# Kernel optimization log

Measured on AMD Instinct MI355X. Metric: run time of the kernel, lower is better.

## Reference

```python
import jax, jax.numpy as jnp
import numpy as np

N_QUBITS = 12   # data qubits; device has 3*n wires but ancillas provably stay in a product state
N_LAYERS = 6
BATCH = 768


def _apply_1q(state, gate, wire):
    """state: (B,)+(2,)*n complex; gate: (2,2) shared or (B,2,2) per-sample."""
    state = jnp.moveaxis(state, 1 + wire, -1)
    if gate.ndim == 3:
        state = jnp.einsum('b...i,bji->b...j', state, gate)
    else:
        state = jnp.einsum('b...i,ji->b...j', state, gate)
    return jnp.moveaxis(state, -1, 1 + wire)


def _apply_cnot(state, control, target):
    state = jnp.moveaxis(state, (1 + control, 1 + target), (-2, -1))
    state = jnp.stack([state[..., 0, :], state[..., 1, ::-1]], axis=-2)
    return jnp.moveaxis(state, (-2, -1), (1 + control, 1 + target))


def _forward(x, params):
    B, n = x.shape
    dim = 2 ** n
    state = jnp.zeros((B, dim), jnp.complex64).at[:, 0].set(1.0)
    state = state.reshape((B,) + (2,) * n)
    # angle embedding: RX(x[:, i]) on data qubit i (per-sample batched gates)
    c = jnp.cos(x / 2).astype(jnp.complex64)          # (B, n)
    s = (-1j * jnp.sin(x / 2)).astype(jnp.complex64)  # (B, n)
    for i in range(n):
        g = jnp.stack([jnp.stack([c[:, i], s[:, i]], -1),
                       jnp.stack([s[:, i], c[:, i]], -1)], -2)  # (B,2,2)
        state = _apply_1q(state, g, i)
    # variational layers: Rot(phi, theta, omega) = RZ(omega) RY(theta) RZ(phi), then CNOT chain
    for l in range(params.shape[0]):
        for q in range(n):
            phi, theta, omega = params[l, q, 0], params[l, q, 1], params[l, q, 2]
            ct, st = jnp.cos(theta / 2), jnp.sin(theta / 2)
            ep = jnp.exp(-0.5j * (phi + omega))   # e^{-i(phi+omega)/2}
            em = jnp.exp(0.5j * (phi - omega))    # e^{ i(phi-omega)/2}
            g = jnp.stack([jnp.stack([ep * ct, -em * st]),
                           jnp.stack([jnp.conj(em) * st, jnp.conj(ep) * ct])])
        
            state = _apply_1q(state, g, q)
        for q in range(n - 1):
            state = _apply_cnot(state, q, q + 1)
    # <Z_i> for each data qubit via a single probs @ signs matmul
    probs = jnp.abs(state.reshape(B, dim)) ** 2
    bits = (jnp.arange(dim)[:, None] >> jnp.arange(n - 1, -1, -1)[None, :]) & 1
    signs = (1.0 - 2.0 * bits).astype(probs.dtype)     # (dim, n)
    exps = probs @ signs                               # (B, n)
    # readout-error mitigation: calibration matrix from ideal simulator SPAM runs
    # (ideal <Z_j> for basis state with qubit i flipped -> (Z+1)/2 = ones - eye)
    M = jnp.ones((n, n), probs.dtype) - jnp.eye(n, dtype=probs.dtype)
    calib = jnp.linalg.pinv(M)
    mitigated = ((exps + 1.0) * 0.5) @ calib.T
    return 2.0 * mitigated - 1.0


def setup_inputs() -> dict:
    key = jax.random.key(0)
    k1, k2 = jax.random.split(key)
    x = jax.random.normal(k1, (BATCH, N_QUBITS), jnp.float32)
    params = jax.random.normal(k2, (N_LAYERS, N_QUBITS, 3), jnp.float32)
    return {"x": x, "params": params}


def reference(x, params):
    return _forward(x, params)
```

## Files before the change

### kernel.cpp

```cpp
#include <hip/hip_runtime.h>

#define NQ 12
#define DIM 4096
#define NL 6
#define THREADS 512
#define BATCH 768

struct M12 { unsigned c[12]; };
constexpr unsigned mapv(const M12& m, unsigned v) {
    unsigned r = 0;
    for (int i = 0; i < 12; ++i) if ((v >> i) & 1) r ^= m.c[i];
    return r;
}
constexpr M12 ident() { M12 m{}; for (int i = 0; i < 12; ++i) m.c[i] = 1u << i; return m; }
constexpr M12 mmul(const M12& a, const M12& b) { M12 r{}; for (int i = 0; i < 12; ++i) r.c[i] = mapv(a, b.c[i]); return r; }
constexpr M12 Gmat()  { M12 m{}; for (int i = 0; i < 12; ++i) m.c[i] = (1u << i) | (i ? (1u << (i - 1)) : 0u); return m; }
constexpr M12 Gimat() { M12 m{}; for (int i = 0; i < 12; ++i) m.c[i] = (2u << i) - 1u; return m; }
constexpr M12 Tmat()  { M12 m = ident(); for (int i = 0; i < 3; ++i) { m.c[i] = 1u << (9 + i); m.c[9 + i] = 1u << i; } return m; }
constexpr M12 Gpow(int n)  { M12 r = ident(); for (int i = 0; i < n; ++i) r = mmul(Gmat(),  r); return r; }
constexpr M12 Gipow(int n) { M12 r = ident(); for (int i = 0; i < n; ++i) r = mmul(Gimat(), r); return r; }
constexpr M12 Lam(int k)    { return (k & 1) ? mmul(Gpow(k - 1), Tmat()) : Gpow(k); }
constexpr M12 LamInv(int k) { return (k & 1) ? mmul(Tmat(), Gipow(k - 1)) : Gipow(k); }
constexpr int par(unsigned v) { int c = 0; for (int b = 0; b < 12; ++b) c ^= (v >> b) & 1; return c; }
constexpr unsigned mask_of(int lam, int p, int k) { return mapv(LamInv(k), mapv(Gpow(lam), 1u << p)); }
constexpr unsigned role_of(int lam, int p, int k) {
    unsigned f = 0;
    for (int b = 0; b < 12; ++b)
        if ((mapv(Gipow(lam), mapv(Lam(k), 1u << b)) >> p) & 1) f |= 1u << b;
    return f;
}
constexpr unsigned kap(unsigned h) { return ((h & 7u) << 9) | (h >> 3); }
struct Off8  { unsigned v[8]; };
struct Col12 { unsigned v[12]; };
constexpr Off8 offs_of(int k) {
    M12 R = mmul(LamInv(k - 1), Lam(k));
    Off8 o{};
    for (unsigned j = 0; j < 8; ++j) o.v[j] = kap(mapv(R, j));
    return o;
}
constexpr Col12 cols_of(int k) {
    M12 R = mmul(LamInv(k - 1), Lam(k));
    Col12 c{};
    for (int i = 0; i < 12; ++i) c.v[i] = kap(mapv(R, 1u << i));
    return c;
}

__device__ __forceinline__ float2 crow(float2 c0, float2 a, float2 c1, float2 b) {
    float2 r;
    r.x = c0.x * a.x - c0.y * a.y + c1.x * b.x - c1.y * b.y;
    r.y = c0.x * a.y + c0.y * a.x + c1.x * b.y + c1.y * b.x;
    return r;
}
template<int CTRL> __device__ __forceinline__ float dppf(float v) {
    return __int_as_float(__builtin_amdgcn_update_dpp(0, __float_as_int(v), CTRL, 0xF, 0xF, true));
}
template<int XM> __device__ __forceinline__ float bxf(float v) {
    if constexpr (XM == 1)      return dppf<0xB1>(v);
    else if constexpr (XM == 2) return dppf<0x4E>(v);
    else if constexpr (XM == 3) return dppf<0x1B>(v);
    else if constexpr (XM < 32) return __int_as_float(__builtin_amdgcn_ds_swizzle(__float_as_int(v), (XM << 10) | 0x1F));
    else                        return __shfl_xor(v, XM, 64);
}
template<int XM> __device__ __forceinline__ float2 bx2(float2 v) { return make_float2(bxf<XM>(v.x), bxf<XM>(v.y)); }

template<int LAM, int P, int K>
__device__ __forceinline__ void pass(float2 (&amp)[8], const float* __restrict__ gw, const int lane) {
    constexpr unsigned MU = mask_of(LAM, P, K);
    constexpr unsigned FV = role_of(LAM, P, K);
    static_assert(MU != 0 && (MU >> 9) == 0, "mask touches wave bits");
    static_assert((FV >> 9) == 0, "role touches wave bits");
    static_assert(par(MU & FV) == 1, "pair not split by role");
    constexpr int MJ = MU & 7, ML = (int)(MU >> 3);
    constexpr int FJ = FV & 7, FL = (int)(FV >> 3);
    constexpr int GI = (LAM * NQ + (11 - P)) * 8;
    const float2 g00 = make_float2(gw[GI + 0], gw[GI + 1]);
    const float2 g01 = make_float2(gw[GI + 2], gw[GI + 3]);
    const float2 g10 = make_float2(gw[GI + 4], gw[GI + 5]);
    const float2 g11 = make_float2(gw[GI + 6], gw[GI + 7]);
    if constexpr (ML == 0) {
        float2 Oda = g00, Ooa = g01, Odb = g11, Oob = g10;
        if constexpr (FL != 0) {
            const bool lf = (__popc(lane & FL) & 1) != 0;
            Oda = lf ? g11 : g00; Ooa = lf ? g10 : g01;
            Odb = lf ? g00 : g11; Oob = lf ? g01 : g10;
        }
        #pragma unroll
        for (int j = 0; j < 8; ++j) {
            if ((__builtin_popcount((unsigned)(FJ & j)) & 1) == 0) {
                const int jb = j ^ MJ;
                const float2 a = amp[j], b = amp[jb];
                amp[j]  = crow(Oda, a, Ooa, b);
                amp[jb] = crow(Odb, b, Oob, a);
            }
        }
    } else {
        float2 pv[8];
        #pragma unroll
        for (int j = 0; j < 8; ++j) pv[j] = bx2<ML>(amp[j ^ MJ]);
        if constexpr (FL == 0) {
            #pragma unroll
            for (int j = 0; j < 8; ++j) {
                constexpr_bool_hack:;
                const bool r = (__builtin_popcount((unsigned)(FJ & j)) & 1) != 0;
                amp[j] = crow(r ? g11 : g00, amp[j], r ? g10 : g01, pv[j]);
            }
        } else {
            const bool lf = (__popc(lane & FL) & 1) != 0;
            const float2 O0d = lf ? g11 : g00, O0o = lf ? g10 : g01;
            const float2 O1d = lf ? g00 : g11, O1o = lf ? g01 : g10;
            #pragma unroll
            for (int j = 0; j < 8; ++j) {
                const bool r = (__builtin_popcount((unsigned)(FJ & j)) & 1) != 0;
                amp[j] = crow(r ? O1d : O0d, amp[j], r ? O1o : O0o, pv[j]);
            }
        }
    }
}

template<int K>
__device__ __forceinline__ unsigned tbase(const int tid) {
    constexpr Col12 C = cols_of(K);
    unsigned r = 0;
    #pragma unroll
    for (int i = 3; i < 12; ++i)
        if ((tid >> (i - 3)) & 1) r ^= C.v[i];
    return r;
}
template<int K>
__device__ __forceinline__ void transit(float2 (&amp)[8], float2* __restrict__ st,
                                        const int tid, const unsigned baseT, const unsigned baseG) {
    if constexpr (K > 1) __syncthreads();
    #pragma unroll
    for (int j = 0; j < 8; ++j) st[(j << 9) | tid] = amp[j];
    __syncthreads();
    constexpr Off8 OF = offs_of(K);
    const unsigned base = (K & 1) ? baseT : baseG;
    #pragma unroll
    for (int j = 0; j < 8; ++j) amp[j] = st[base ^ OF.v[j]];
}

template<int B>
__device__ __forceinline__ void rstage(float& v, float (&D)[6], float& a9, float& a10, float& a11) {
    constexpr int XM = 1 << B;
    const float sv = bxf<XM>(v);
    D[B] = v - sv;
    v += sv;
    #pragma unroll
    for (int c = 0; c < B; ++c) D[c] += bxf<XM>(D[c]);
    a9 += bxf<XM>(a9); a10 += bxf<XM>(a10); a11 += bxf<XM>(a11);
}

__global__ void setup_kernel(const float* __restrict__ x, const float* __restrict__ params,
                             float* __restrict__ ws) {
    const int t = blockIdx.x * 256 + threadIdx.x;
    if (t < NL * NQ) {
        const float phi = params[t * 3 + 0], th = params[t * 3 + 1], om = params[t * 3 + 2];
        float ct, stt, ca, sa, cb, sb;
        __sincosf(0.5f * th, &stt, &ct);
        __sincosf(0.5f * (phi + om), &sa, &ca);
        __sincosf(0.5f * (phi - om), &sb, &cb);
        float* g = ws + t * 8;
        g[0] =  ca * ct;  g[1] = -sa * ct;
        g[2] = -cb * stt; g[3] = -sb * stt;
        g[4] =  cb * stt; g[5] = -sb * stt;
        g[6] =  ca * ct;  g[7] =  sa * ct;
    }
    if (t < BATCH * NQ) {
        const int bb = t / NQ, i = t - bb * NQ;
        float s, c;
        __sincosf(0.5f * x[t], &s, &c);
        ws[1024 + bb * 32 + i]      = c;
        ws[1024 + bb * 32 + 16 + i] = s;
    }
}

__global__ __launch_bounds__(THREADS, 6)
void qsim_kernel(const float* __restrict__ ws, float* __restrict__ out) {
    __shared__ float2 st[DIM];
    __shared__ float red[8 * 10];
    __shared__ float ev[NQ];

    const int b = blockIdx.x;
    const int tid = threadIdx.x;
    const int lane = tid & 63;
    const int wave = tid >> 6;
    const float* __restrict__ gw = ws;
    const float* __restrict__ cs = ws + 1024 + b * 32;

    const unsigned baseT = tbase<1>(tid);
    const unsigned baseG = tbase<2>(tid);

    float rt = 1.0f;
    #pragma unroll
    for (int i = 0; i < 9; ++i) {
        const bool bit = (tid >> (8 - i)) & 1;
        rt *= bit ? cs[16 + i] : cs[i];
    }
    const int pt = __popc((unsigned)tid & 0x1FFu);
    float2 amp[8];
    #pragma unroll
    for (int j = 0; j < 8; ++j) {
        float v = rt;
        v *= (j & 4) ? cs[16 + 9]  : cs[9];
        v *= (j & 2) ? cs[16 + 10] : cs[10];
        v *= (j & 1) ? cs[16 + 11] : cs[11];
        const int ph = (pt + __builtin_popcount((unsigned)j)) & 3;
        amp[j].x = (ph == 0) ? v : (ph == 2) ? -v : 0.0f;
        amp[j].y = (ph == 1) ? -v : (ph == 3) ? v : 0.0f;
    }

    pass<0,0,0>(amp, gw, lane); pass<0,1,0>(amp, gw, lane); pass<0,2,0>(amp, gw, lane);
    pass<0,3,0>(amp, gw, lane); pass<0,4,0>(amp, gw, lane); pass<0,5,0>(amp, gw, lane);
    pass<0,6,0>(amp, gw, lane); pass<0,7,0>(amp, gw, lane); pass<0,8,0>(amp, gw, lane);
    transit<1>(amp, st, tid, baseT, baseG);
    pass<0,9,1>(amp, gw, lane); pass<0,10,1>(amp, gw, lane); pass<0,11,1>(amp, gw, lane);
    pass<1,11,1>(amp, gw, lane); pass<1,10,1>(amp, gw, lane); pass<1,9,1>(amp, gw, lane);
    pass<1,8,1>(amp, gw, lane);  pass<1,7,1>(amp, gw, lane);  pass<1,6,1>(amp, gw, lane);
    pass<1,5,1>(amp, gw, lane);  pass<1,4,1>(amp, gw, lane);
    transit<2>(amp, st, tid, baseT, baseG);
    pass<1,0,2>(amp, gw, lane); pass<1,1,2>(amp, gw, lane); pass<1,2,2>(amp, gw, lane); pass<1,3,2>(amp, gw, lane);
    pass<2,0,2>(amp, gw, lane); pass<2,1,2>(amp, gw, lane); pass<2,2,2>(amp, gw, lane);
    pass<2,3,2>(amp, gw, lane); pass<2,4,2>(amp, gw, lane); pass<2,5,2>(amp, gw, lane);
    pass<2,6,2>(amp, gw, lane); pass<2,7,2>(amp, gw, lane); pass<2,8,2>(amp, gw, lane);
    transit<3>(amp, st, tid, baseT, baseG);
    pass<2,9,3>(amp, gw, lane); pass<2,10,3>(amp, gw, lane); pass<2,11,3>(amp, gw, lane);
    pass<3,11,3>(amp, gw, lane); pass<3,10,3>(amp, gw, lane); pass<3,9,3>(amp, gw, lane);
    pass<3,8,3>(amp, gw, lane);  pass<3,7,3>(amp, gw, lane);  pass<3,6,3>(amp, gw, lane);
    pass<3,5,3>(amp, gw, lane);  pass<3,4,3>(amp, gw, lane);
    transit<4>(amp, st, tid, baseT, baseG);
    pass<3,0,4>(amp, gw, lane); pass<3,1,4>(amp, gw, lane); pass<3,2,4>(amp, gw, lane); pass<3,3,4>(amp, gw, lane);
    pass<4,0,4>(amp, gw, lane); pass<4,1,4>(amp, gw, lane); pass<4,2,4>(amp, gw, lane);
    pass<4,3,4>(amp, gw, lane); pass<4,4,4>(amp, gw, lane); pass<4,5,4>(amp, gw, lane);
    pass<4,6,4>(amp, gw, lane); pass<4,7,4>(amp, gw, lane); pass<4,8,4>(amp, gw, lane);
    transit<5>(amp, st, tid, baseT, baseG);
    pass<4,9,5>(amp, gw, lane); pass<4,10,5>(amp, gw, lane); pass<4,11,5>(amp, gw, lane);
    pass<5,11,5>(amp, gw, lane); pass<5,10,5>(amp, gw, lane); pass<5,9,5>(amp, gw, lane);
    pass<5,8,5>(amp, gw, lane);  pass<5,7,5>(amp, gw, lane);  pass<5,6,5>(amp, gw, lane);
    pass<5,5,5>(amp, gw, lane);  pass<5,4,5>(amp, gw, lane);
    transit<6>(amp, st, tid, baseT, baseG);
    pass<5,0,6>(amp, gw, lane); pass<5,1,6>(amp, gw, lane); pass<5,2,6>(amp, gw, lane); pass<5,3,6>(amp, gw, lane);

    float p8[8];
    #pragma unroll
    for (int j = 0; j < 8; ++j) p8[j] = amp[j].x * amp[j].x + amp[j].y * amp[j].y;
    const float t01 = p8[0] + p8[1], d01 = p8[0] - p8[1];
    const float t23 = p8[2] + p8[3], d23 = p8[2] - p8[3];
    const float t45 = p8[4] + p8[5], d45 = p8[4] - p8[5];
    const float t67 = p8[6] + p8[7], d67 = p8[6] - p8[7];
    const float s03 = t01 + t23, s47 = t45 + t67;
    float S   = s03 + s47;
    float a11 = (d01 + d23) + (d45 + d67);
    float a10 = (t01 - t23) + (t45 - t67);
    float a9  = s03 - s47;
    float D[6];
    rstage<0>(S, D, a9, a10, a11); rstage<1>(S, D, a9, a10, a11);
    rstage<2>(S, D, a9, a10, a11); rstage<3>(S, D, a9, a10, a11);
    rstage<4>(S, D, a9, a10, a11); rstage<5>(S, D, a9, a10, a11);
    if (lane == 0) {
        float* rw = red + wave * 10;
        rw[0] = S;
        #pragma unroll
        for (int c = 0; c < 6; ++c) rw[1 + c] = D[c];
        rw[7] = a9; rw[8] = a10; rw[9] = a11;
    }
    __syncthreads();
    if (tid < NQ) {
        float e = 0.0f;
        #pragma unroll
        for (int w = 0; w < 8; ++w) {
            const float* rw = red + w * 10;
            float s;
            if (tid == 0)      s = ((w >> 2) & 1) ? -rw[0] : rw[0];
            else if (tid == 1) s = ((w >> 1) & 1) ? -rw[0] : rw[0];
            else if (tid == 2) s = ((w >> 0) & 1) ? -rw[0] : rw[0];
            else if (tid < 9)  s = rw[1 + (8 - tid)];
            else               s = rw[7 + (tid - 9)];
            e += s;
        }
        ev[tid] = e;
    }
    __syncthreads();
    if (tid < NQ) {
        float Sm = 0.0f;
        #pragma unroll
        for (int i = 0; i < NQ; ++i) Sm += ev[i];
        out[b * NQ + tid] = (Sm + 12.0f) * (1.0f / 11.0f) - ev[tid] - 2.0f;
    }
}

extern "C" void kernel_launch(void* const* d_in, const int* in_sizes, int n_in,
                              void* d_out, int out_size, void* d_ws, size_t ws_size,
                              hipStream_t stream) {
    const float* x      = (const float*)d_in[0];
    const float* params = (const float*)d_in[1];
    float* ws  = (float*)d_ws;
    float* out = (float*)d_out;
    setup_kernel<<<dim3(36), dim3(256), 0, stream>>>(x, params, ws);
    qsim_kernel<<<dim3(BATCH), dim3(THREADS), 0, stream>>>(ws, out);
}
```

Baseline: 106.0 us.

## Restructure simulator to 256 threads with 16 amplitudes each and packed-FP32 gates

Switches the per-sample statevector kernel from 512 threads holding 8 amplitudes to 256 threads holding 16. A new qubit-permutation schedule lets each half-layer apply 4 gates in registers and 2 via DPP lane swaps, with one shared-memory transpose between half-layers. Complex amplitudes are packed as doubles and multiplied with v_pk_mul/v_pk_fma inline assembly. The shared-memory layout gets an XOR swizzle to reduce bank conflicts. This aims to cut shuffle, LDS and sync overhead per gate, but raises register pressure (launch bounds go from 6 to 4) and leaves fewer waves per block.

```diff
diff --git a/kernel.cpp b/kernel.cpp
--- a/kernel.cpp
+++ b/kernel.cpp
@@ -3,7 +3,7 @@
 #define NQ 12
 #define DIM 4096
 #define NL 6
-#define THREADS 512
+#define THREADS 256
 #define BATCH 768
 
 struct M12 { unsigned c[12]; };
@@ -16,40 +16,102 @@
 constexpr M12 mmul(const M12& a, const M12& b) { M12 r{}; for (int i = 0; i < 12; ++i) r.c[i] = mapv(a, b.c[i]); return r; }
 constexpr M12 Gmat()  { M12 m{}; for (int i = 0; i < 12; ++i) m.c[i] = (1u << i) | (i ? (1u << (i - 1)) : 0u); return m; }
 constexpr M12 Gimat() { M12 m{}; for (int i = 0; i < 12; ++i) m.c[i] = (2u << i) - 1u; return m; }
-constexpr M12 Tmat()  { M12 m = ident(); for (int i = 0; i < 3; ++i) { m.c[i] = 1u << (9 + i); m.c[9 + i] = 1u << i; } return m; }
-constexpr M12 Gpow(int n)  { M12 r = ident(); for (int i = 0; i < n; ++i) r = mmul(Gmat(),  r); return r; }
-constexpr M12 Gipow(int n) { M12 r = ident(); for (int i = 0; i < n; ++i) r = mmul(Gimat(), r); return r; }
-constexpr M12 Lam(int k)    { return (k & 1) ? mmul(Gpow(k - 1), Tmat()) : Gpow(k); }
-constexpr M12 LamInv(int k) { return (k & 1) ? mmul(Tmat(), Gipow(k - 1)) : Gipow(k); }
-constexpr int par(unsigned v) { int c = 0; for (int b = 0; b < 12; ++b) c ^= (v >> b) & 1; return c; }
-constexpr unsigned mask_of(int lam, int p, int k) { return mapv(LamInv(k), mapv(Gpow(lam), 1u << p)); }
+constexpr M12 Smat()  { M12 m{}; for (int i = 0; i < 12; ++i) m.c[i] = (i < 6) ? (1u << (i + 6)) : (1u << (i - 6)); return m; }
+struct Pow7 { M12 p[7]; };
+constexpr Pow7 mkpow(const M12 g) { Pow7 t{}; t.p[0] = ident(); for (int i = 1; i < 7; ++i) t.p[i] = mmul(g, t.p[i - 1]); return t; }
+constexpr Pow7 GP  = mkpow(Gmat());
+constexpr Pow7 GIP = mkpow(Gimat());
+struct LamT { M12 l[13]; };
+constexpr LamT mklam() {
+    LamT t{};
+    for (int k = 0; k < 12; ++k) t.l[k] = (k & 1) ? GP.p[k >> 1] : mmul(GP.p[k >> 1], Smat());
+    t.l[12] = GP.p[6];
+    return t;
+}
+constexpr LamT mklami() {
+    LamT t{};
+    for (int k = 0; k < 12; ++k) t.l[k] = (k & 1) ? GIP.p[k >> 1] : mmul(Smat(), GIP.p[k >> 1]);
+    t.l[12] = GIP.p[6];
+    return t;
+}
+constexpr LamT LAMT  = mklam();
+constexpr LamT LAMIT = mklami();
+constexpr bool eqm(const M12& a, const M12& b) { for (int i = 0; i < 12; ++i) if (a.c[i] != b.c[i]) return false; return true; }
+constexpr unsigned mask_of(int lam, int p, int k) { return mapv(LAMIT.l[k], mapv(GP.p[lam], 1u << p)); }
 constexpr unsigned role_of(int lam, int p, int k) {
     unsigned f = 0;
     for (int b = 0; b < 12; ++b)
-        if ((mapv(Gipow(lam), mapv(Lam(k), 1u << b)) >> p) & 1) f |= 1u << b;
+        if ((mapv(GIP.p[lam], mapv(LAMT.l[k], 1u << b)) >> p) & 1) f |= 1u << b;
     return f;
 }
-constexpr unsigned kap(unsigned h) { return ((h & 7u) << 9) | (h >> 3); }
-struct Off8  { unsigned v[8]; };
-struct Col12 { unsigned v[12]; };
-constexpr Off8 offs_of(int k) {
-    M12 R = mmul(LamInv(k - 1), Lam(k));
-    Off8 o{};
-    for (unsigned j = 0; j < 8; ++j) o.v[j] = kap(mapv(R, j));
-    return o;
-}
-constexpr Col12 cols_of(int k) {
-    M12 R = mmul(LamInv(k - 1), Lam(k));
-    Col12 c{};
-    for (int i = 0; i < 12; ++i) c.v[i] = kap(mapv(R, 1u << i));
-    return c;
-}
-
-__device__ __forceinline__ float2 crow(float2 c0, float2 a, float2 c1, float2 b) {
-    float2 r;
-    r.x = c0.x * a.x - c0.y * a.y + c1.x * b.x - c1.y * b.y;
-    r.y = c0.x * a.y + c0.y * a.x + c1.x * b.y + c1.y * b.x;
-    return r;
+constexpr bool check_layer(int L) {
+    for (int p = 0; p < 12; ++p) {
+        const int k = (p >= 6) ? 2 * L : 2 * L + 1;
+        const unsigned exp_ = (p >= 6) ? (1u << (p - 6)) : (1u << p);
+        if (mask_of(L, p, k) != exp_) return false;
+        if (role_of(L, p, k) != exp_) return false;
+    }
+    return true;
+}
+static_assert(check_layer(0), "layer0 masks/roles not unit cheap bits");
+static_assert(check_layer(1), "layer1");
+static_assert(check_layer(2), "layer2");
+static_assert(check_layer(3), "layer3");
+static_assert(check_layer(4), "layer4");
+static_assert(check_layer(5), "layer5");
+constexpr M12 Rk(int k) { return mmul(LAMIT.l[k - 1], LAMT.l[k]); }
+constexpr M12 R_S  = Smat();
+constexpr M12 R_GS = mmul(Gmat(), Smat());
+constexpr M12 R_G  = Gmat();
+static_assert(eqm(Rk(1), R_S) && eqm(Rk(3), R_S) && eqm(Rk(11), R_S), "T1 != S");
+static_assert(eqm(Rk(2), R_GS) && eqm(Rk(10), R_GS), "T2 != G*S");
+static_assert(eqm(Rk(12), R_G), "T3 != G");
+
+constexpr unsigned kap(unsigned h) {
+    const unsigned cell = ((h & 15u) << 8) | (h >> 4);
+    return cell ^ ((cell >> 8) & 15u) ^ (((cell >> 6) & 3u) << 4);
+}
+struct Off16 { unsigned v[16]; };
+struct Col8  { unsigned v[8]; };
+constexpr Off16 roff(const M12& R) { Off16 o{}; for (unsigned j = 0; j < 16; ++j) o.v[j] = kap(mapv(R, j)); return o; }
+constexpr Col8  rcol(const M12& R) { Col8 c{}; for (int i = 0; i < 8; ++i) c.v[i] = kap(mapv(R, 1u << (4 + i))); return c; }
+constexpr Off16 OFF_S = roff(R_S), OFF_GS = roff(R_GS), OFF_G = roff(R_G);
+constexpr Col8  COL_S = rcol(R_S), COL_GS = rcol(R_GS), COL_G = rcol(R_G);
+
+__device__ __forceinline__ double pkmul_s(double c, double a) {
+    double r;
+    asm("v_pk_mul_f32 %0, %1, %2 op_sel:[0,0] op_sel_hi:[0,1]\n\t"
+        "v_pk_fma_f32 %0, %1, %2, %0 op_sel:[1,1,0] op_sel_hi:[1,0,1] neg_lo:[1,0,0]"
+        : "=&v"(r) : "s"(c), "v"(a));
+    return r;
+}
+__device__ __forceinline__ double pkfma_s(double c, double a, double d) {
+    double r;
+    asm("v_pk_fma_f32 %0, %1, %2, %3 op_sel:[0,0,0] op_sel_hi:[0,1,1]\n\t"
+        "v_pk_fma_f32 %0, %1, %2, %0 op_sel:[1,1,0] op_sel_hi:[1,0,1] neg_lo:[1,0,0]"
+        : "=&v"(r) : "s"(c), "v"(a), "v"(d));
+    return r;
+}
+__device__ __forceinline__ double pkmul_v(double c, double a) {
+    double r;
+    asm("v_pk_mul_f32 %0, %1, %2 op_sel:[0,0] op_sel_hi:[0,1]\n\t"
+        "v_pk_fma_f32 %0, %1, %2, %0 op_sel:[1,1,0] op_sel_hi:[1,0,1] neg_lo:[1,0,0]"
+        : "=&v"(r) : "v"(c), "v"(a));
+    return r;
+}
+__device__ __forceinline__ double pkfma_v(double c, double a, double d) {
+    double r;
+    asm("v_pk_fma_f32 %0, %1, %2, %3 op_sel:[0,0,0] op_sel_hi:[0,1,1]\n\t"
+        "v_pk_fma_f32 %0, %1, %2, %0 op_sel:[1,1,0] op_sel_hi:[1,0,1] neg_lo:[1,0,0]"
+        : "=&v"(r) : "v"(c), "v"(a), "v"(d));
+    return r;
+}
+
+template<int CTRL>
+__device__ __forceinline__ double dpp64(double v) {
+    const int lo = __builtin_amdgcn_update_dpp(0, __double2loint(v), CTRL, 0xF, 0xF, true);
+    const int hi = __builtin_amdgcn_update_dpp(0, __double2hiint(v), CTRL, 0xF, 0xF, true);
+    return __hiloint2double(hi, lo);
 }
 template<int CTRL> __device__ __forceinline__ float dppf(float v) {
     return __int_as_float(__builtin_amdgcn_update_dpp(0, __float_as_int(v), CTRL, 0xF, 0xF, true));
@@ -57,97 +119,87 @@
 template<int XM> __device__ __forceinline__ float bxf(float v) {
     if constexpr (XM == 1)      return dppf<0xB1>(v);
     else if constexpr (XM == 2) return dppf<0x4E>(v);
-    else if constexpr (XM == 3) return dppf<0x1B>(v);
     else if constexpr (XM < 32) return __int_as_float(__builtin_amdgcn_ds_swizzle(__float_as_int(v), (XM << 10) | 0x1F));
     else                        return __shfl_xor(v, XM, 64);
 }
-template<int XM> __device__ __forceinline__ float2 bx2(float2 v) { return make_float2(bxf<XM>(v.x), bxf<XM>(v.y)); }
-
-template<int LAM, int P, int K>
-__device__ __forceinline__ void pass(float2 (&amp)[8], const float* __restrict__ gw, const int lane) {
-    constexpr unsigned MU = mask_of(LAM, P, K);
-    constexpr unsigned FV = role_of(LAM, P, K);
-    static_assert(MU != 0 && (MU >> 9) == 0, "mask touches wave bits");
-    static_assert((FV >> 9) == 0, "role touches wave bits");
-    static_assert(par(MU & FV) == 1, "pair not split by role");
-    constexpr int MJ = MU & 7, ML = (int)(MU >> 3);
-    constexpr int FJ = FV & 7, FL = (int)(FV >> 3);
-    constexpr int GI = (LAM * NQ + (11 - P)) * 8;
-    const float2 g00 = make_float2(gw[GI + 0], gw[GI + 1]);
-    const float2 g01 = make_float2(gw[GI + 2], gw[GI + 3]);
-    const float2 g10 = make_float2(gw[GI + 4], gw[GI + 5]);
-    const float2 g11 = make_float2(gw[GI + 6], gw[GI + 7]);
-    if constexpr (ML == 0) {
-        float2 Oda = g00, Ooa = g01, Odb = g11, Oob = g10;
-        if constexpr (FL != 0) {
-            const bool lf = (__popc(lane & FL) & 1) != 0;
-            Oda = lf ? g11 : g00; Ooa = lf ? g10 : g01;
-            Odb = lf ? g00 : g11; Oob = lf ? g01 : g10;
+
+template<int RB>
+__device__ __forceinline__ void regpassPK(double (&amp)[16], const double* __restrict__ g) {
+    const double g00 = g[0], g01 = g[1], g10 = g[2], g11 = g[3];
+    #pragma unroll
+    for (int j = 0; j < 16; ++j)
+        if (!(j & (1 << RB))) {
+            const int jb = j | (1 << RB);
+            const double a = amp[j], b2 = amp[jb];
+            amp[j]  = pkfma_s(g01, b2, pkmul_s(g00, a));
+            amp[jb] = pkfma_s(g10, a,  pkmul_s(g11, b2));
         }
-        #pragma unroll
-        for (int j = 0; j < 8; ++j) {
-            if ((__builtin_popcount((unsigned)(FJ & j)) & 1) == 0) {
-                const int jb = j ^ MJ;
-                const float2 a = amp[j], b = amp[jb];
-                amp[j]  = crow(Oda, a, Ooa, b);
-                amp[jb] = crow(Odb, b, Oob, a);
-            }
-        }
-    } else {
-        float2 pv[8];
-        #pragma unroll
-        for (int j = 0; j < 8; ++j) pv[j] = bx2<ML>(amp[j ^ MJ]);
-        if constexpr (FL == 0) {
-            #pragma unroll
-            for (int j = 0; j < 8; ++j) {
-                constexpr_bool_hack:;
-                const bool r = (__builtin_popcount((unsigned)(FJ & j)) & 1) != 0;
-                amp[j] = crow(r ? g11 : g00, amp[j], r ? g10 : g01, pv[j]);
-            }
-        } else {
-            const bool lf = (__popc(lane & FL) & 1) != 0;
-            const float2 O0d = lf ? g11 : g00, O0o = lf ? g10 : g01;
-            const float2 O1d = lf ? g00 : g11, O1o = lf ? g01 : g10;
-            #pragma unroll
-            for (int j = 0; j < 8; ++j) {
-                const bool r = (__builtin_popcount((unsigned)(FJ & j)) & 1) != 0;
-                amp[j] = crow(r ? O1d : O0d, amp[j], r ? O1o : O0o, pv[j]);
-            }
-        }
-    }
-}
-
-template<int K>
-__device__ __forceinline__ unsigned tbase(const int tid) {
-    constexpr Col12 C = cols_of(K);
+}
+template<int XM>
+__device__ __forceinline__ void dpppassPK(double (&amp)[16], const double* __restrict__ g, const int lane) {
+    constexpr int CTRL = (XM == 1) ? 0xB1 : 0x4E;
+    const bool side = (lane & XM) != 0;
+    const double cA = side ? g[3] : g[0];
+    const double cB = side ? g[2] : g[1];
+    #pragma unroll
+    for (int j = 0; j < 16; ++j) {
+        const double r = dpp64<CTRL>(amp[j]);
+        amp[j] = pkfma_v(cB, r, pkmul_v(cA, amp[j]));
+    }
+}
+
+template<int L>
+__device__ __forceinline__ void epochA(double (&amp)[16], const double* __restrict__ gd, const int lane) {
+    const double* gL = gd + L * 48;
+    regpassPK<0>(amp, gL + 5 * 4);
+    regpassPK<1>(amp, gL + 4 * 4);
+    regpassPK<2>(amp, gL + 3 * 4);
+    regpassPK<3>(amp, gL + 2 * 4);
+    dpppassPK<1>(amp, gL + 1 * 4, lane);
+    dpppassPK<2>(amp, gL + 0 * 4, lane);
+}
+template<int L>
+__device__ __forceinline__ void epochB(double (&amp)[16], const double* __restrict__ gd, const int lane) {
+    const double* gL = gd + L * 48;
+    regpassPK<0>(amp, gL + 11 * 4);
+    regpassPK<1>(amp, gL + 10 * 4);
+    regpassPK<2>(amp, gL +  9 * 4);
+    regpassPK<3>(amp, gL +  8 * 4);
+    dpppassPK<1>(amp, gL + 7 * 4, lane);
+    dpppassPK<2>(amp, gL + 6 * 4, lane);
+}
+
+template<int RSEL, bool FIRST>
+__device__ __forceinline__ void transit(double (&amp)[16], double* __restrict__ st,
+                                        const unsigned wbase, const unsigned rbase) {
+    if constexpr (!FIRST) __syncthreads();
+    #pragma unroll
+    for (int j = 0; j < 16; ++j)
+        st[wbase ^ (unsigned)((j << 8) ^ j)] = amp[j];
+    __syncthreads();
+    constexpr Off16 OF = (RSEL == 0) ? OFF_S : (RSEL == 1) ? OFF_GS : OFF_G;
+    #pragma unroll
+    for (int j = 0; j < 16; ++j) amp[j] = st[rbase ^ OF.v[j]];
+}
+template<int RSEL>
+__device__ __forceinline__ unsigned rbase_of(const int tid) {
+    constexpr Col8 C = (RSEL == 0) ? COL_S : (RSEL == 1) ? COL_GS : COL_G;
     unsigned r = 0;
     #pragma unroll
-    for (int i = 3; i < 12; ++i)
-        if ((tid >> (i - 3)) & 1) r ^= C.v[i];
-    return r;
-}
-template<int K>
-__device__ __forceinline__ void transit(float2 (&amp)[8], float2* __restrict__ st,
-                                        const int tid, const unsigned baseT, const unsigned baseG) {
-    if constexpr (K > 1) __syncthreads();
-    #pragma unroll
-    for (int j = 0; j < 8; ++j) st[(j << 9) | tid] = amp[j];
-    __syncthreads();
-    constexpr Off8 OF = offs_of(K);
-    const unsigned base = (K & 1) ? baseT : baseG;
-    #pragma unroll
-    for (int j = 0; j < 8; ++j) amp[j] = st[base ^ OF.v[j]];
+    for (int i = 0; i < 8; ++i) if ((tid >> i) & 1) r ^= C.v[i];
+    return r;
 }
 
 template<int B>
-__device__ __forceinline__ void rstage(float& v, float (&D)[6], float& a9, float& a10, float& a11) {
+__device__ __forceinline__ void rstage(float& S, float (&D)[6], float (&Bv)[4]) {
     constexpr int XM = 1 << B;
-    const float sv = bxf<XM>(v);
-    D[B] = v - sv;
-    v += sv;
+    const float sv = bxf<XM>(S);
+    D[B] = S - sv;
+    S += sv;
     #pragma unroll
     for (int c = 0; c < B; ++c) D[c] += bxf<XM>(D[c]);
-    a9 += bxf<XM>(a9); a10 += bxf<XM>(a10); a11 += bxf<XM>(a11);
+    #pragma unroll
+    for (int q = 0; q < 4; ++q) Bv[q] += bxf<XM>(Bv[q]);
 }
 
 __global__ void setup_kernel(const float* __restrict__ x, const float* __restrict__ params,
@@ -174,107 +226,101 @@
     }
 }
 
-__global__ __launch_bounds__(THREADS, 6)
+__global__ __launch_bounds__(THREADS, 4)
 void qsim_kernel(const float* __restrict__ ws, float* __restrict__ out) {
-    __shared__ float2 st[DIM];
-    __shared__ float red[8 * 10];
+    __shared__ double st[DIM];
+    __shared__ float red[4 * 11];
     __shared__ float ev[NQ];
 
     const int b = blockIdx.x;
     const int tid = threadIdx.x;
     const int lane = tid & 63;
     const int wave = tid >> 6;
-    const float* __restrict__ gw = ws;
-    const float* __restrict__ cs = ws + 1024 + b * 32;
-
-    const unsigned baseT = tbase<1>(tid);
-    const unsigned baseG = tbase<2>(tid);
+    const double* __restrict__ gd = (const double*)ws;
+    const float*  __restrict__ cs = ws + 1024 + b * 32;
+
+    const unsigned wbase = (unsigned)tid ^ (((unsigned)tid & 0xC0u) >> 2);
+    const unsigned rbS  = rbase_of<0>(tid);
+    const unsigned rbGS = rbase_of<1>(tid);
+    const unsigned rbG  = rbase_of<2>(tid);
 
     float rt = 1.0f;
-    #pragma unroll
-    for (int i = 0; i < 9; ++i) {
-        const bool bit = (tid >> (8 - i)) & 1;
-        rt *= bit ? cs[16 + i] : cs[i];
-    }
-    const int pt = __popc((unsigned)tid & 0x1FFu);
-    float2 amp[8];
-    #pragma unroll
-    for (int j = 0; j < 8; ++j) {
+    rt *= ((tid >> 1) & 1) ? cs[16 + 0]  : cs[0];
+    rt *= ((tid >> 0) & 1) ? cs[16 + 1]  : cs[1];
+    rt *= ((tid >> 7) & 1) ? cs[16 + 6]  : cs[6];
+    rt *= ((tid >> 6) & 1) ? cs[16 + 7]  : cs[7];
+    rt *= ((tid >> 5) & 1) ? cs[16 + 8]  : cs[8];
+    rt *= ((tid >> 4) & 1) ? cs[16 + 9]  : cs[9];
+    rt *= ((tid >> 3) & 1) ? cs[16 + 10] : cs[10];
+    rt *= ((tid >> 2) & 1) ? cs[16 + 11] : cs[11];
+    const int pt = __popc((unsigned)tid & 0xFFu);
+
+    double amp[16];
+    #pragma unroll
+    for (int j = 0; j < 16; ++j) {
         float v = rt;
-        v *= (j & 4) ? cs[16 + 9]  : cs[9];
-        v *= (j & 2) ? cs[16 + 10] : cs[10];
-        v *= (j & 1) ? cs[16 + 11] : cs[11];
+        v *= (j & 8) ? cs[16 + 2] : cs[2];
+        v *= (j & 4) ? cs[16 + 3] : cs[3];
+        v *= (j & 2) ? cs[16 + 4] : cs[4];
+        v *= (j & 1) ? cs[16 + 5] : cs[5];
         const int ph = (pt + __builtin_popcount((unsigned)j)) & 3;
-        amp[j].x = (ph == 0) ? v : (ph == 2) ? -v : 0.0f;
-        amp[j].y = (ph == 1) ? -v : (ph == 3) ? v : 0.0f;
-    }
-
-    pass<0,0,0>(amp, gw, lane); pass<0,1,0>(amp, gw, lane); pass<0,2,0>(amp, gw, lane);
-    pass<0,3,0>(amp, gw, lane); pass<0,4,0>(amp, gw, lane); pass<0,5,0>(amp, gw, lane);
-    pass<0,6,0>(amp, gw, lane); pass<0,7,0>(amp, gw, lane); pass<0,8,0>(amp, gw, lane);
-    transit<1>(amp, st, tid, baseT, baseG);
-    pass<0,9,1>(amp, gw, lane); pass<0,10,1>(amp, gw, lane); pass<0,11,1>(amp, gw, lane);
-    pass<1,11,1>(amp, gw, lane); pass<1,10,1>(amp, gw, lane); pass<1,9,1>(amp, gw, lane);
-    pass<1,8,1>(amp, gw, lane);  pass<1,7,1>(amp, gw, lane);  pass<1,6,1>(amp, gw, lane);
-    pass<1,5,1>(amp, gw, lane);  pass<1,4,1>(amp, gw, lane);
-    transit<2>(amp, st, tid, baseT, baseG);
-    pass<1,0,2>(amp, gw, lane); pass<1,1,2>(amp, gw, lane); pass<1,2,2>(amp, gw, lane); pass<1,3,2>(amp, gw, lane);
-    pass<2,0,2>(amp, gw, lane); pass<2,1,2>(amp, gw, lane); pass<2,2,2>(amp, gw, lane);
-    pass<2,3,2>(amp, gw, lane); pass<2,4,2>(amp, gw, lane); pass<2,5,2>(amp, gw, lane);
-    pass<2,6,2>(amp, gw, lane); pass<2,7,2>(amp, gw, lane); pass<2,8,2>(amp, gw, lane);
-    transit<3>(amp, st, tid, baseT, baseG);
-    pass<2,9,3>(amp, gw, lane); pass<2,10,3>(amp, gw, lane); pass<2,11,3>(amp, gw, lane);
-    pass<3,11,3>(amp, gw, lane); pass<3,10,3>(amp, gw, lane); pass<3,9,3>(amp, gw, lane);
-    pass<3,8,3>(amp, gw, lane);  pass<3,7,3>(amp, gw, lane);  pass<3,6,3>(amp, gw, lane);
-    pass<3,5,3>(amp, gw, lane);  pass<3,4,3>(amp, gw, lane);
-    transit<4>(amp, st, tid, baseT, baseG);
-    pass<3,0,4>(amp, gw, lane); pass<3,1,4>(amp, gw, lane); pass<3,2,4>(amp, gw, lane); pass<3,3,4>(amp, gw, lane);
-    pass<4,0,4>(amp, gw, lane); pass<4,1,4>(amp, gw, lane); pass<4,2,4>(amp, gw, lane);
-    pass<4,3,4>(amp, gw, lane); pass<4,4,4>(amp, gw, lane); pass<4,5,4>(amp, gw, lane);
-    pass<4,6,4>(amp, gw, lane); pass<4,7,4>(amp, gw, lane); pass<4,8,4>(amp, gw, lane);
-    transit<5>(amp, st, tid, baseT, baseG);
-    pass<4,9,5>(amp, gw, lane); pass<4,10,5>(amp, gw, lane); pass<4,11,5>(amp, gw, lane);
-    pass<5,11,5>(amp, gw, lane); pass<5,10,5>(amp, gw, lane); pass<5,9,5>(amp, gw, lane);
-    pass<5,8,5>(amp, gw, lane);  pass<5,7,5>(amp, gw, lane);  pass<5,6,5>(amp, gw, lane);
-    pass<5,5,5>(amp, gw, lane);  pass<5,4,5>(amp, gw, lane);
-    transit<6>(amp, st, tid, baseT, baseG);
-    pass<5,0,6>(amp, gw, lane); pass<5,1,6>(amp, gw, lane); pass<5,2,6>(amp, gw, lane); pass<5,3,6>(amp, gw, lane);
-
-    float p8[8];
-    #pragma unroll
-    for (int j = 0; j < 8; ++j) p8[j] = amp[j].x * amp[j].x + amp[j].y * amp[j].y;
-    const float t01 = p8[0] + p8[1], d01 = p8[0] - p8[1];
-    const float t23 = p8[2] + p8[3], d23 = p8[2] - p8[3];
-    const float t45 = p8[4] + p8[5], d45 = p8[4] - p8[5];
-    const float t67 = p8[6] + p8[7], d67 = p8[6] - p8[7];
-    const float s03 = t01 + t23, s47 = t45 + t67;
-    float S   = s03 + s47;
-    float a11 = (d01 + d23) + (d45 + d67);
-    float a10 = (t01 - t23) + (t45 - t67);
-    float a9  = s03 - s47;
+        const float re = (ph == 0) ? v : (ph == 2) ? -v : 0.0f;
+        const float im = (ph == 1) ? -v : (ph == 3) ? v : 0.0f;
+        amp[j] = __hiloint2double(__float_as_int(im), __float_as_int(re));
+    }
+
+    epochA<0>(amp, gd, lane); transit<0, true >(amp, st, wbase, rbS);
+    epochB<0>(amp, gd, lane); transit<1, false>(amp, st, wbase, rbGS);
+    epochA<1>(amp, gd, lane); transit<0, false>(amp, st, wbase, rbS);
+    epochB<1>(amp, gd, lane); transit<1, false>(amp, st, wbase, rbGS);
+    epochA<2>(amp, gd, lane); transit<0, false>(amp, st, wbase, rbS);
+    epochB<2>(amp, gd, lane); transit<1, false>(amp, st, wbase, rbGS);
+    epochA<3>(amp, gd, lane); transit<0, false>(amp, st, wbase, rbS);
+    epochB<3>(amp, gd, lane); transit<1, false>(amp, st, wbase, rbGS);
+    epochA<4>(amp, gd, lane); transit<0, false>(amp, st, wbase, rbS);
+    epochB<4>(amp, gd, lane); transit<1, false>(amp, st, wbase, rbGS);
+    epochA<5>(amp, gd, lane); transit<0, false>(amp, st, wbase, rbS);
+    epochB<5>(amp, gd, lane); transit<2, false>(amp, st, wbase, rbG);
+
+    float p16[16];
+    #pragma unroll
+    for (int j = 0; j < 16; ++j) {
+        const float re = __int_as_float(__double2loint(amp[j]));
+        const float im = __int_as_float(__double2hiint(amp[j]));
+        p16[j] = re * re + im * im;
+    }
+    float e8[8], B0 = 0.0f;
+    #pragma unroll
+    for (int i = 0; i < 8; ++i) { e8[i] = p16[2*i] + p16[2*i+1]; B0 += p16[2*i] - p16[2*i+1]; }
+    float f4[4], B1 = 0.0f;
+    #pragma unroll
+    for (int i = 0; i < 4; ++i) { f4[i] = e8[2*i] + e8[2*i+1]; B1 += e8[2*i] - e8[2*i+1]; }
+    const float h0 = f4[0] + f4[1], h1 = f4[2] + f4[3];
+    const float B2 = (f4[0] - f4[1]) + (f4[2] - f4[3]);
+    float S = h0 + h1;
+    float Bv[4] = { B0, B1, B2, h0 - h1 };
     float D[6];
-    rstage<0>(S, D, a9, a10, a11); rstage<1>(S, D, a9, a10, a11);
-    rstage<2>(S, D, a9, a10, a11); rstage<3>(S, D, a9, a10, a11);
-    rstage<4>(S, D, a9, a10, a11); rstage<5>(S, D, a9, a10, a11);
+    rstage<0>(S, D, Bv); rstage<1>(S, D, Bv); rstage<2>(S, D, Bv);
+    rstage<3>(S, D, Bv); rstage<4>(S, D, Bv); rstage<5>(S, D, Bv);
     if (lane == 0) {
-        float* rw = red + wave * 10;
+        float* rw = red + wave * 11;
         rw[0] = S;
         #pragma unroll
         for (int c = 0; c < 6; ++c) rw[1 + c] = D[c];
-        rw[7] = a9; rw[8] = a10; rw[9] = a11;
+        #pragma unroll
+        for (int q = 0; q < 4; ++q) rw[7 + q] = Bv[q];
     }
     __syncthreads();
     if (tid < NQ) {
         float e = 0.0f;
         #pragma unroll
-        for (int w = 0; w < 8; ++w) {
-            const float* rw = red + w * 10;
+        for (int w = 0; w < 4; ++w) {
+            const float* rw = red + w * 11;
             float s;
-            if (tid == 0)      s = ((w >> 2) & 1) ? -rw[0] : rw[0];
-            else if (tid == 1) s = ((w >> 1) & 1) ? -rw[0] : rw[0];
-            else if (tid == 2) s = ((w >> 0) & 1) ? -rw[0] : rw[0];
-            else if (tid < 9)  s = rw[1 + (8 - tid)];
-            else               s = rw[7 + (tid - 9)];
+            if (tid == 0)      s = ((w >> 1) & 1) ? -rw[0] : rw[0];
+            else if (tid == 1) s = ((w >> 0) & 1) ? -rw[0] : rw[0];
+            else if (tid < 8)  s = rw[1 + (7 - tid)];
+            else               s = rw[7 + (11 - tid)];
             e += s;
         }
         ev[tid] = e;
```

Measured after the change: 96.26 us. 1.1x faster.
